# Performance work log

Measured on AMD Instinct MI355X. Metric: run time of the kernel, lower is better.

Reference implementation:

```python
import jax, jax.numpy as jnp
import numpy as np

F_, H_, W_ = 6, 16, 28          # latent video grid (frames, height, width)
DIM, NH = 1536, 12
HD = DIM // NH                   # 128
L = F_ * H_ * W_                 # 2688 tokens
EPS = 1e-6
BLOCK = 3 * H_ * W_              # block_causal_size = 3*frame_height*frame_width


def setup_inputs() -> dict:
    key = jax.random.key(0)
    ks = jax.random.split(key, 8)
    def lin(k):
        return jax.random.normal(k, (DIM, DIM), jnp.float32) * 0.02
    x = jax.random.normal(ks[0], (1, L, DIM), jnp.float32)
    # RoPE freqs: unit-modulus complex numbers stored as [...,(re,im)]
    ang = jax.random.uniform(ks[1], (1024, HD // 2), jnp.float32, -np.pi, np.pi)
    freqs = jnp.stack([jnp.cos(ang), jnp.sin(ang)], axis=-1)  # [1024, 64, 2]
    return {
        'x': x,
        'seq_lens': jnp.array([L], jnp.int32),
        'grid_sizes': jnp.array([[F_, H_, W_]], jnp.int32),
        'freqs': freqs,
        'Wq': lin(ks[2]), 'bq': jnp.zeros((DIM,), jnp.float32),
        'Wk': lin(ks[3]), 'bk': jnp.zeros((DIM,), jnp.float32),
        'Wv': lin(ks[4]), 'bv': jnp.zeros((DIM,), jnp.float32),
        'Wo': lin(ks[5]), 'bo': jnp.zeros((DIM,), jnp.float32),
        'gq': jnp.ones((DIM,), jnp.float32),
        'gk': jnp.ones((DIM,), jnp.float32),
    }


def _rmsnorm(x, g):
    # WanRMSNorm: x * rsqrt(mean(x^2) + eps) * weight
    return x * jax.lax.rsqrt(jnp.mean(x * x, axis=-1, keepdims=True) + EPS) * g


def _rope_apply(x, F, H, W, freqs, start_frame=0):
    # x: [B, L, n, d]; freqs: [1024, d//2, 2] (re, im). Per-axis split [c0, c3, c3].
    B, Lx, n, d = x.shape
    c = d // 2
    c3 = c // 3
    c0 = c - 2 * c3
    f0 = freqs[start_frame:start_frame + F, :c0]      # [F, c0, 2]
    f1 = freqs[:H, c0:c0 + c3]                        # [H, c3, 2]
    f2 = freqs[:W, c0 + c3:]                          # [W, c3, 2]
    ff = jnp.concatenate([
        jnp.broadcast_to(f0[:, None, None], (F, H, W, c0, 2)),
        jnp.broadcast_to(f1[None, :, None], (F, H, W, c3, 2)),
        jnp.broadcast_to(f2[None, None, :], (F, H, W, c3, 2)),
    ], axis=3).reshape(Lx, 1, c, 2)                   # [L, 1, c, 2]
    xr = x.reshape(B, Lx, n, c, 2)
    xre, xim = xr[..., 0], xr[..., 1]
    fre, fim = ff[None, ..., 0], ff[None, ..., 1]     # broadcast over batch, heads
    ore = xre * fre - xim * fim
    oim = xre * fim + xim * fre
    return jnp.stack([ore, oim], axis=-1).reshape(B, Lx, n, d)


def reference(x, seq_lens, grid_sizes, freqs, Wq, bq, Wk, bk, Wv, bv, Wo, bo, gq, gk):
    b, s = x.shape[:2]
    F = int(grid_sizes[0, 0]); H = int(grid_sizes[0, 1]); W = int(grid_sizes[0, 2])
    q = _rmsnorm(x @ Wq + bq, gq).reshape(b, s, NH, HD)
    k = _rmsnorm(x @ Wk + bk, gk).reshape(b, s, NH, HD)
    v = (x @ Wv + bv).reshape(b, s, NH, HD)
    rq = _rope_apply(q, F, H, W, freqs)
    rk = _rope_apply(k, F, H, W, freqs)
    # block-causal attention: query attends to keys in same-or-earlier 3-frame block
    scores = jnp.einsum('bihd,bjhd->bhij', rq, rk) * (HD ** -0.5)
    blk = jnp.arange(s) // (3 * H * W)
    mask = blk[None, :] <= blk[:, None]               # [s, s]
    scores = jnp.where(mask[None, None], scores, -1e30)
    attn = jax.nn.softmax(scores, axis=-1)
    out = jnp.einsum('bhij,bjhd->bihd', attn, v).reshape(b, s, DIM)
    return out @ Wo + bo
```

## Files before the change

kernel.cpp:

```cpp
#include <hip/hip_runtime.h>

#define L_SEQ 2688
#define DIM   1536
#define NH    12
#define HD    128
#define BLK_TOK 1344
#define HW_   448
#define W_    28

typedef unsigned short u16;
typedef unsigned int   u32;
typedef __attribute__((ext_vector_type(4))) float f32x4;
typedef __attribute__((ext_vector_type(16))) float f32x16;
typedef __attribute__((ext_vector_type(8))) short s16x8;
typedef __attribute__((ext_vector_type(2))) int i32x2;
typedef __attribute__((ext_vector_type(4))) u32 u32x4;

__device__ __forceinline__ u16 f2b(float f) {
    u32 u = __builtin_bit_cast(u32, f);
    return (u16)((u + 0x7FFFu + ((u >> 16) & 1u)) >> 16);
}
__device__ __forceinline__ float b2f(u16 b) {
    return __builtin_bit_cast(float, (u32)b << 16);
}
__device__ __forceinline__ u32 cvt_pk_bf16(float lo, float hi) {
    u32 r;
    asm("v_cvt_pk_bf16_f32 %0, %1, %2" : "=v"(r) : "v"(lo), "v"(hi));
    return r;
}

__global__ __launch_bounds__(256) void k_cvt_x(const float* __restrict__ x,
                                               u16* __restrict__ xb, int n4) {
    int i = blockIdx.x * 256 + threadIdx.x;
    int stride = gridDim.x * 256;
    for (; i < n4; i += stride) {
        float4 v = ((const float4*)x)[i];
        ushort4 o;
        o.x = f2b(v.x); o.y = f2b(v.y); o.z = f2b(v.z); o.w = f2b(v.w);
        ((ushort4*)xb)[i] = o;
    }
}

__global__ __launch_bounds__(256) void k_trans_w(const float* __restrict__ w0,
                                                 const float* __restrict__ w1,
                                                 const float* __restrict__ w2,
                                                 const float* __restrict__ w3,
                                                 u16* __restrict__ wt_all) {
    const float* w = blockIdx.z == 0 ? w0 : blockIdx.z == 1 ? w1 : blockIdx.z == 2 ? w2 : w3;
    u16* wt = wt_all + (size_t)blockIdx.z * DIM * DIM;
    __shared__ float t[64][65];
    const int k0 = blockIdx.y * 64, n0 = blockIdx.x * 64;
    const int c = threadIdx.x & 63, rg = threadIdx.x >> 6;
#pragma unroll
    for (int it = 0; it < 16; ++it) {
        int r = rg * 16 + it;
        t[r][c] = w[(size_t)(k0 + r) * DIM + n0 + c];
    }
    __syncthreads();
#pragma unroll
    for (int it = 0; it < 16; ++it) {
        int r = rg * 16 + it;
        wt[(size_t)(n0 + r) * DIM + k0 + c] = f2b(t[c][r]);
    }
}

template<int OUTF>
__global__ __launch_bounds__(256, 2) void k_gemm(const u16* __restrict__ A,
                                                 const u16* __restrict__ Bt_all,
                                                 const float* __restrict__ b0,
                                                 const float* __restrict__ b1,
                                                 const float* __restrict__ b2,
                                                 void* __restrict__ out_all) {
    const int z = blockIdx.z;
    const u16* Bt = Bt_all + (size_t)z * DIM * DIM;
    const float* bias = z == 0 ? b0 : z == 1 ? b1 : b2;

    __shared__ u16 lA[128 * 32];
    __shared__ u16 lB[128 * 32];
    const int tid = threadIdx.x, lane = tid & 63, wid = tid >> 6;
    const int wm = wid >> 1, wn = wid & 1;
    const int bm = blockIdx.y, bn = blockIdx.x;
    const int lr = lane & 15, lg = lane >> 4;

    f32x4 acc[4][4] = {};

    for (int kt = 0; kt < DIM / 32; ++kt) {
#pragma unroll
        for (int i = 0; i < 2; ++i) {
            int s = wid * 128 + i * 64 + lane;
            int row = s >> 2, c16 = s & 3;
            const u16* ga = A + (size_t)(bm * 128 + row) * DIM + kt * 32 + c16 * 8;
            __builtin_amdgcn_global_load_lds(
                (const __attribute__((address_space(1))) u32*)ga,
                (__attribute__((address_space(3))) u32*)&lA[(wid * 128 + i * 64) * 8],
                16, 0, 0);
            const u16* gb = Bt + (size_t)(bn * 128 + row) * DIM + kt * 32 + c16 * 8;
            __builtin_amdgcn_global_load_lds(
                (const __attribute__((address_space(1))) u32*)gb,
                (__attribute__((address_space(3))) u32*)&lB[(wid * 128 + i * 64) * 8],
                16, 0, 0);
        }
        __syncthreads();
        s16x8 af[4], bf[4];
#pragma unroll
        for (int m = 0; m < 4; ++m)
            af[m] = *(const s16x8*)&lA[(wm * 64 + m * 16 + lr) * 32 + lg * 8];
#pragma unroll
        for (int n = 0; n < 4; ++n)
            bf[n] = *(const s16x8*)&lB[(wn * 64 + n * 16 + lr) * 32 + lg * 8];
#pragma unroll
        for (int m = 0; m < 4; ++m)
#pragma unroll
            for (int n = 0; n < 4; ++n)
                acc[m][n] = __builtin_amdgcn_mfma_f32_16x16x32_bf16(af[m], bf[n], acc[m][n], 0, 0, 0);
        __syncthreads();
    }
#pragma unroll
    for (int n = 0; n < 4; ++n) {
        int col = bn * 128 + wn * 64 + n * 16 + lr;
        float bv = bias[col];
#pragma unroll
        for (int m = 0; m < 4; ++m) {
            int row0 = bm * 128 + wm * 64 + m * 16 + lg * 4;
#pragma unroll
            for (int r = 0; r < 4; ++r) {
                float v = acc[m][n][r] + bv;
                if (OUTF)
                    ((float*)out_all)[(size_t)(row0 + r) * DIM + col] = v;
                else
                    ((u16*)out_all)[(size_t)z * L_SEQ * DIM + (size_t)(row0 + r) * DIM + col] = f2b(v);
            }
        }
    }
}

__global__ __launch_bounds__(256) void k_norm_rope(const u16* __restrict__ pre_all,
                                                   const float* __restrict__ gq,
                                                   const float* __restrict__ gk,
                                                   const float* __restrict__ freqs,
                                                   u16* __restrict__ qh,
                                                   u16* __restrict__ kh) {
    const int which = blockIdx.y;
    const u16* pre = pre_all + (size_t)which * L_SEQ * DIM;
    const float* g = which ? gk : gq;
    u16* outh = which ? kh : qh;

    const int i = blockIdx.x;
    const int t = threadIdx.x;
    const u32* prow = (const u32*)(pre + (size_t)i * DIM);

    float re[3], im[3];
    float ss = 0.f;
#pragma unroll
    for (int a = 0; a < 3; ++a) {
        u32 p = prow[t + a * 256];
        float x = b2f((u16)(p & 0xFFFFu)), y = b2f((u16)(p >> 16));
        re[a] = x; im[a] = y;
        ss += x * x + y * y;
    }
#pragma unroll
    for (int o = 32; o > 0; o >>= 1) ss += __shfl_down(ss, o, 64);
    __shared__ float sred[4];
    if ((t & 63) == 0) sred[t >> 6] = ss;
    __syncthreads();
    float rms = rsqrtf((sred[0] + sred[1] + sred[2] + sred[3]) * (1.0f / DIM) + 1e-6f);

    const int f = i / HW_;
    const int rem = i - f * HW_;
    const int hp = rem / W_;
    const int wp = rem - hp * W_;
#pragma unroll
    for (int a = 0; a < 3; ++a) {
        int j = t + a * 256;
        int h = j >> 6, pj = j & 63;
        float2 gg = ((const float2*)g)[j];
        float x = re[a] * rms * gg.x;
        float y = im[a] * rms * gg.y;
        int ridx = pj < 22 ? f : (pj < 43 ? hp : wp);
        float2 cs = ((const float2*)freqs)[ridx * 64 + pj];
        float ore = x * cs.x - y * cs.y;
        float oim = x * cs.y + y * cs.x;
        u32 o = (u32)f2b(ore) | ((u32)f2b(oim) << 16);
        ((u32*)outh)[(size_t)h * (L_SEQ * 64) + (size_t)i * 64 + pj] = o;
    }
}

__global__ __launch_bounds__(256) void k_vtrans(const u16* __restrict__ vpre,
                                                u16* __restrict__ vt) {
    const int i0 = blockIdx.x * 64, d0 = blockIdx.y * 64, h = blockIdx.z;
    __shared__ u16 t[64][68];
    const int c = threadIdx.x & 63, rg = threadIdx.x >> 6;
#pragma unroll
    for (int it = 0; it < 16; ++it) {
        int r = rg * 16 + it;
        t[r][c] = vpre[(size_t)(i0 + r) * DIM + h * HD + d0 + c];
    }
    __syncthreads();
#pragma unroll
    for (int it = 0; it < 16; ++it) {
        int r = rg * 16 + it;
        vt[(size_t)h * (HD * L_SEQ) + (size_t)(d0 + r) * L_SEQ + i0 + c] = t[c][r];
    }
}

__global__ __launch_bounds__(256, 2) void k_attn(const u16* __restrict__ qh,
                                                 const u16* __restrict__ kh,
                                                 const u16* __restrict__ vt,
                                                 u16* __restrict__ ob,
                                                 float* __restrict__ Opart,
                                                 float* __restrict__ mlp) {
    __shared__ char lsm[2][32768];

    const int flat = blockIdx.x;
    const int xcd = flat & 7, idx = flat >> 3;
    const int work = (xcd < 4) ? (xcd * 95 + idx) : (380 + (xcd - 4) * 94 + idx);
    const int head = work / 63;
    const int bx = work - head * 63;
    int qt, kv0, mode;
    if (bx < 21)      { qt = bx;      kv0 = 0;  mode = 0; }
    else if (bx < 42) { qt = bx;      kv0 = 0;  mode = 1; }
    else              { qt = bx - 21; kv0 = 21; mode = 2; }

    const int tid = threadIdx.x, lane = tid & 63, w = tid >> 6;
    const int pairI = w >> 1;
    const int qhalf = w & 1;
    const int q31 = lane & 31, hi = lane >> 5;
    const size_t hOff = (size_t)head * ((size_t)L_SEQ * HD);
    const u16* Kh = kh + hOff;
    const u16* Vh = vt + hOff;
    const int qrow0 = qt * 64 + qhalf * 32;

    s16x8 aq[8];
#pragma unroll
    for (int kk = 0; kk < 8; ++kk)
        aq[kk] = *(const s16x8*)&qh[hOff + (size_t)(qrow0 + q31) * HD + kk * 16 + hi * 8];

    const int pt = tid & 127;
    const int rh = pt >> 4, ck = pt & 15;
    const int rv = pt >> 3, cvv = pt & 7;
    char* slot = lsm[pairI];

    f32x16 acc[4] = {};
    float mrun = -1e30f, lrun = 0.f;
    const float sc2 = 0.12751739646917983f;

    for (int it = 0; it < 11; ++it) {
        const int mytile = 2 * it + pairI;
        const bool active = mytile < 21;
        if (active) {
            const int tg = kv0 + mytile;
#pragma unroll
            for (int i = 0; i < 8; ++i) {
                const u16* src = Kh + (size_t)(tg * 64 + i * 8 + rh) * HD + 8 * (ck ^ ((i & 1) * 8 + rh));
                __builtin_amdgcn_global_load_lds(
                    (const __attribute__((address_space(1))) u32*)src,
                    (__attribute__((address_space(3))) u32*)(slot + i * 2048 + pt * 16), 16, 0, 0);
            }
#pragma unroll
            for (int i = 0; i < 8; ++i) {
                const u16* src = Vh + (size_t)(i * 16 + rv) * L_SEQ + tg * 64 + 8 * (cvv ^ (rv & 7));
                __builtin_amdgcn_global_load_lds(
                    (const __attribute__((address_space(1))) u32*)src,
                    (__attribute__((address_space(3))) u32*)(slot + 16384 + i * 2048 + pt * 16), 16, 0, 0);
            }
        }
        __syncthreads();
        if (active) {
            f32x16 sv[2] = {};
            __builtin_amdgcn_s_setprio(1);
#pragma unroll
            for (int js = 0; js < 2; ++js)
#pragma unroll
                for (int kk = 0; kk < 8; ++kk) {
                    int off = (js * 32 + q31) * 256 + ((kk * 32 + hi * 16) ^ ((q31 & 15) << 4));
                    s16x8 kf = *(const s16x8*)(slot + off);
                    sv[js] = __builtin_amdgcn_mfma_f32_32x32x16_bf16(kf, aq[kk], sv[js], 0, 0, 0);
                }
            __builtin_amdgcn_s_setprio(0);

            float mx = fmaxf(sv[0][0], sv[1][0]);
#pragma unroll
            for (int e = 1; e < 16; ++e) mx = fmaxf(mx, fmaxf(sv[0][e], sv[1][e]));
            mx = fmaxf(mx, __shfl_xor(mx, 32, 64));
            mx *= sc2;
            const int resc = (mx - mrun) > 11.5f;
            const float mm = resc ? mx : mrun;
            const float fac = resc ? __builtin_amdgcn_exp2f(mrun - mm) : 1.0f;
            mrun = mm;
            float sum = 0.f;
#pragma unroll
            for (int js = 0; js < 2; ++js)
#pragma unroll
                for (int e = 0; e < 16; ++e) {
                    float pv = __builtin_amdgcn_exp2f(sv[js][e] * sc2 - mm);
                    sv[js][e] = pv;
                    sum += pv;
                }
            sum += __shfl_xor(sum, 32, 64);
            lrun = lrun * fac + sum;
            if (__any(resc)) {
#pragma unroll
                for (int ds = 0; ds < 4; ++ds)
#pragma unroll
                    for (int e = 0; e < 16; ++e) acc[ds][e] *= fac;
            }

            s16x8 pa[4];
#pragma unroll
            for (int js = 0; js < 2; ++js)
#pragma unroll
                for (int hf = 0; hf < 2; ++hf) {
                    u32 a0 = cvt_pk_bf16(sv[js][hf * 8 + 0], sv[js][hf * 8 + 1]);
                    u32 a1 = cvt_pk_bf16(sv[js][hf * 8 + 2], sv[js][hf * 8 + 3]);
                    u32 b0 = cvt_pk_bf16(sv[js][hf * 8 + 4], sv[js][hf * 8 + 5]);
                    u32 b1 = cvt_pk_bf16(sv[js][hf * 8 + 6], sv[js][hf * 8 + 7]);
                    i32x2 r0 = __builtin_amdgcn_permlane32_swap((int)a0, (int)b0, false, false);
                    i32x2 r1 = __builtin_amdgcn_permlane32_swap((int)a1, (int)b1, false, false);
                    u32x4 fw;
                    fw.x = (u32)r0.x; fw.y = (u32)r1.x; fw.z = (u32)r0.y; fw.w = (u32)r1.y;
                    pa[js * 2 + hf] = __builtin_bit_cast(s16x8, fw);
                }

            __builtin_amdgcn_s_setprio(1);
#pragma unroll
            for (int jstep = 0; jstep < 4; ++jstep)
#pragma unroll
                for (int ds = 0; ds < 4; ++ds) {
                    int off = 16384 + (ds * 32 + q31) * 128 + ((jstep * 32 + hi * 16) ^ ((q31 & 7) << 4));
                    s16x8 vf = *(const s16x8*)(slot + off);
                    acc[ds] = __builtin_amdgcn_mfma_f32_32x32x16_bf16(vf, pa[jstep], acc[ds], 0, 0, 0);
                }
            __builtin_amdgcn_s_setprio(0);
        }
        __syncthreads();
    }

    float2* mlb = (float2*)(lsm[1]);
    char* accb = lsm[0];
    if (w >= 2) {
        char* base = accb + qhalf * 16384 + lane * 256;
#pragma unroll
        for (int ds = 0; ds < 4; ++ds)
#pragma unroll
            for (int g = 0; g < 4; ++g) {
                f32x4 v4;
#pragma unroll
                for (int e = 0; e < 4; ++e) v4[e] = acc[ds][g * 4 + e];
                *(f32x4*)(base + (((ds * 4 + g) * 16) ^ ((lane & 15) << 4))) = v4;
            }
        if (hi == 0) {
            float2 t2; t2.x = mrun; t2.y = lrun;
            mlb[qhalf * 32 + q31] = t2;
        }
    }
    __syncthreads();
    if (w < 2) {
        float2 ml2 = mlb[qhalf * 32 + q31];
        float M = fmaxf(mrun, ml2.x);
        float wa = exp2f(mrun - M), wb = exp2f(ml2.x - M);
        lrun = lrun * wa + ml2.y * wb;
        mrun = M;
        const char* base = accb + qhalf * 16384 + lane * 256;
#pragma unroll
        for (int ds = 0; ds < 4; ++ds)
#pragma unroll
            for (int g = 0; g < 4; ++g) {
                f32x4 v4 = *(const f32x4*)(base + (((ds * 4 + g) * 16) ^ ((lane & 15) << 4)));
#pragma unroll
                for (int e = 0; e < 4; ++e) acc[ds][g * 4 + e] = acc[ds][g * 4 + e] * wa + v4[e] * wb;
            }
        if (mode == 0) {
            const float inv = 1.0f / lrun;
            u16* orow = ob + (size_t)(qrow0 + q31) * DIM + head * HD;
#pragma unroll
            for (int ds = 0; ds < 4; ++ds)
#pragma unroll
                for (int g = 0; g < 4; ++g) {
                    uint2 pk2;
                    pk2.x = cvt_pk_bf16(acc[ds][g * 4 + 0] * inv, acc[ds][g * 4 + 1] * inv);
                    pk2.y = cvt_pk_bf16(acc[ds][g * 4 + 2] * inv, acc[ds][g * 4 + 3] * inv);
                    *(uint2*)(orow + ds * 32 + g * 8 + hi * 4) = pk2;
                }
        } else {
            const int pairo = (head * 21 + (qt - 21)) * 2 + (mode - 1);
            float* Op = Opart + (size_t)pairo * (64 * 128);
            const int rowl = qhalf * 32 + q31;
#pragma unroll
            for (int ds = 0; ds < 4; ++ds)
#pragma unroll
                for (int g = 0; g < 4; ++g) {
                    float4 v4;
                    v4.x = acc[ds][g * 4 + 0]; v4.y = acc[ds][g * 4 + 1];
                    v4.z = acc[ds][g * 4 + 2]; v4.w = acc[ds][g * 4 + 3];
                    *(float4*)(&Op[rowl * 128 + ds * 32 + g * 8 + hi * 4]) = v4;
                }
            if (hi == 0) {
                float2 t2; t2.x = mrun; t2.y = lrun;
                ((float2*)mlp)[(size_t)pairo * 64 + rowl] = t2;
            }
        }
    }
}

__global__ __launch_bounds__(256) void k_merge(const float* __restrict__ Opart,
                                               const float* __restrict__ mlp,
                                               u16* __restrict__ ob) {
    const int b = blockIdx.x;
    const int qt2 = b % 21, head = b / 21;
    const int pair = head * 21 + qt2;
    const float* O0 = Opart + (size_t)pair * 2 * 8192;
    const float* O1 = O0 + 8192;
    const int tid = threadIdx.x;
    const int row = tid >> 2, cs = (tid & 3) * 32;
    float2 a = ((const float2*)mlp)[(size_t)pair * 2 * 64 + row];
    float2 c = ((const float2*)mlp)[(size_t)(pair * 2 + 1) * 64 + row];
    float M = fmaxf(a.x, c.x);
    float w0 = exp2f(a.x - M), w1 = exp2f(c.x - M);
    float inv = 1.0f / (w0 * a.y + w1 * c.y);
    w0 *= inv; w1 *= inv;
    const int rowg = BLK_TOK + qt2 * 64 + row;
    u32* orow = (u32*)(ob + (size_t)rowg * DIM + head * HD + cs);
    const float4* p0 = (const float4*)(O0 + row * 128 + cs);
    const float4* p1 = (const float4*)(O1 + row * 128 + cs);
#pragma unroll
    for (int u = 0; u < 8; ++u) {
        float4 x0 = p0[u], x1 = p1[u];
        float o0 = x0.x * w0 + x1.x * w1;
        float o1 = x0.y * w0 + x1.y * w1;
        float o2 = x0.z * w0 + x1.z * w1;
        float o3 = x0.w * w0 + x1.w * w1;
        orow[u * 2]     = (u32)f2b(o0) | ((u32)f2b(o1) << 16);
        orow[u * 2 + 1] = (u32)f2b(o2) | ((u32)f2b(o3) << 16);
    }
}

extern "C" void kernel_launch(void* const* d_in, const int* in_sizes, int n_in,
                              void* d_out, int out_size, void* d_ws, size_t ws_size,
                              hipStream_t stream) {
    const float* x     = (const float*)d_in[0];
    const float* freqs = (const float*)d_in[3];
    const float* Wq    = (const float*)d_in[4];
    const float* bq    = (const float*)d_in[5];
    const float* Wk    = (const float*)d_in[6];
    const float* bk    = (const float*)d_in[7];
    const float* Wv    = (const float*)d_in[8];
    const float* bv    = (const float*)d_in[9];
    const float* Wo    = (const float*)d_in[10];
    const float* bo    = (const float*)d_in[11];
    const float* gq    = (const float*)d_in[12];
    const float* gk    = (const float*)d_in[13];

    const size_t LD = (size_t)L_SEQ * DIM;
    u16* wt_all  = (u16*)d_ws;
    u16* xb      = wt_all + (size_t)4 * DIM * DIM;
    u16* pre_all = xb + LD;
    u16* qh      = pre_all + 3 * LD;
    u16* kh2     = qh + LD;
    u16* vt      = kh2 + LD;
    u16* ob      = vt + LD;
    float* Opart = (float*)pre_all;
    float* mlp   = Opart + (size_t)12 * 21 * 2 * 64 * 128;

    k_cvt_x<<<2016, 256, 0, stream>>>(x, xb, (int)(LD / 4));
    k_trans_w<<<dim3(24, 24, 4), 256, 0, stream>>>(Wq, Wk, Wv, Wo, wt_all);
    k_gemm<0><<<dim3(12, 21, 3), 256, 0, stream>>>(xb, wt_all, bq, bk, bv, pre_all);
    k_norm_rope<<<dim3(L_SEQ, 2), 256, 0, stream>>>(pre_all, gq, gk, freqs, qh, kh2);
    k_vtrans<<<dim3(42, 2, NH), 256, 0, stream>>>(pre_all + 2 * LD, vt);
    k_attn<<<dim3(756), 256, 0, stream>>>(qh, kh2, vt, ob, Opart, mlp);
    k_merge<<<dim3(252), 256, 0, stream>>>(Opart, mlp, ob);
    k_gemm<1><<<dim3(12, 21, 1), 256, 0, stream>>>(ob, wt_all + (size_t)3 * DIM * DIM, bo, bo, bo, d_out);
}
```

Baseline: 173.7 us.

## Process two query tiles per attention workgroup to reuse K/V tiles

Restructures the attention kernel so each workgroup handles two 64-row query tiles, with each wave computing 64 query rows (two 32-row halves) against every K/V tile it loads into LDS. This halves the number of workgroups and the K/V global-to-LDS traffic per query. In exchange it doubles accumulator and Q fragment register pressure per wave, and with 11 pairs per context the last pair has an idle half. The grid shrinks to 396 blocks, which may leave CUs underused.

```diff
diff --git a/kernel.cpp b/kernel.cpp
--- a/kernel.cpp
+++ b/kernel.cpp
@@ -203,6 +203,51 @@
     }
 }
 
+__device__ __forceinline__ void softmax_pack(f32x16* sv, float& mrun, float& lrun,
+                                             f32x16* acc, s16x8* pa) {
+    const float sc2 = 0.12751739646917983f;
+    float mx = fmaxf(sv[0][0], sv[1][0]);
+#pragma unroll
+    for (int e = 1; e < 16; ++e) mx = fmaxf(mx, fmaxf(sv[0][e], sv[1][e]));
+    mx = fmaxf(mx, __shfl_xor(mx, 32, 64));
+    mx *= sc2;
+    const int resc = (mx - mrun) > 11.5f;
+    const float mm = resc ? mx : mrun;
+    const float fac = resc ? __builtin_amdgcn_exp2f(mrun - mm) : 1.0f;
+    mrun = mm;
+    float sum = 0.f;
+#pragma unroll
+    for (int js = 0; js < 2; ++js)
+#pragma unroll
+        for (int e = 0; e < 16; ++e) {
+            float pv = __builtin_amdgcn_exp2f(sv[js][e] * sc2 - mm);
+            sv[js][e] = pv;
+            sum += pv;
+        }
+    sum += __shfl_xor(sum, 32, 64);
+    lrun = lrun * fac + sum;
+    if (__any(resc)) {
+#pragma unroll
+        for (int ds = 0; ds < 4; ++ds)
+#pragma unroll
+            for (int e = 0; e < 16; ++e) acc[ds][e] *= fac;
+    }
+#pragma unroll
+    for (int js = 0; js < 2; ++js)
+#pragma unroll
+        for (int hf = 0; hf < 2; ++hf) {
+            u32 a0 = cvt_pk_bf16(sv[js][hf * 8 + 0], sv[js][hf * 8 + 1]);
+            u32 a1 = cvt_pk_bf16(sv[js][hf * 8 + 2], sv[js][hf * 8 + 3]);
+            u32 b0 = cvt_pk_bf16(sv[js][hf * 8 + 4], sv[js][hf * 8 + 5]);
+            u32 b1 = cvt_pk_bf16(sv[js][hf * 8 + 6], sv[js][hf * 8 + 7]);
+            i32x2 r0 = __builtin_amdgcn_permlane32_swap((int)a0, (int)b0, false, false);
+            i32x2 r1 = __builtin_amdgcn_permlane32_swap((int)a1, (int)b1, false, false);
+            u32x4 fw;
+            fw.x = (u32)r0.x; fw.y = (u32)r1.x; fw.z = (u32)r0.y; fw.w = (u32)r1.y;
+            pa[js * 2 + hf] = __builtin_bit_cast(s16x8, fw);
+        }
+}
+
 __global__ __launch_bounds__(256, 2) void k_attn(const u16* __restrict__ qh,
                                                  const u16* __restrict__ kh,
                                                  const u16* __restrict__ vt,
@@ -210,44 +255,48 @@
                                                  float* __restrict__ Opart,
                                                  float* __restrict__ mlp) {
     __shared__ char lsm[2][32768];
+    __shared__ float2 mlb2[2][64];
 
     const int flat = blockIdx.x;
     const int xcd = flat & 7, idx = flat >> 3;
-    const int work = (xcd < 4) ? (xcd * 95 + idx) : (380 + (xcd - 4) * 94 + idx);
-    const int head = work / 63;
-    const int bx = work - head * 63;
-    int qt, kv0, mode;
-    if (bx < 21)      { qt = bx;      kv0 = 0;  mode = 0; }
-    else if (bx < 42) { qt = bx;      kv0 = 0;  mode = 1; }
-    else              { qt = bx - 21; kv0 = 21; mode = 2; }
+    const int work = (xcd < 4) ? (xcd * 50 + idx) : (200 + (xcd - 4) * 49 + idx);
+    const int head = work / 33;
+    const int rem = work - head * 33;
+    const int ctx = rem / 11, p = rem - (rem / 11) * 11;
+    const int qbase = (ctx == 0) ? 0 : 21;
+    const int kv0 = (ctx == 2) ? 21 : 0;
+    const int mode = ctx;
 
     const int tid = threadIdx.x, lane = tid & 63, w = tid >> 6;
-    const int pairI = w >> 1;
-    const int qhalf = w & 1;
+    const int P = w >> 1, S = w & 1;
     const int q31 = lane & 31, hi = lane >> 5;
+    const int qt = qbase + 2 * p + S;
+    const bool qvalid = (2 * p + S) < 21;
+
     const size_t hOff = (size_t)head * ((size_t)L_SEQ * HD);
     const u16* Kh = kh + hOff;
     const u16* Vh = vt + hOff;
-    const int qrow0 = qt * 64 + qhalf * 32;
-
-    s16x8 aq[8];
-#pragma unroll
-    for (int kk = 0; kk < 8; ++kk)
-        aq[kk] = *(const s16x8*)&qh[hOff + (size_t)(qrow0 + q31) * HD + kk * 16 + hi * 8];
+
+    s16x8 aq0[8], aq1[8];
+    const u16* qp = qh + hOff + (size_t)(qt * 64 + q31) * HD + hi * 8;
+#pragma unroll
+    for (int kk = 0; kk < 8; ++kk) {
+        aq0[kk] = *(const s16x8*)(qp + kk * 16);
+        aq1[kk] = *(const s16x8*)(qp + (size_t)32 * HD + kk * 16);
+    }
 
     const int pt = tid & 127;
     const int rh = pt >> 4, ck = pt & 15;
     const int rv = pt >> 3, cvv = pt & 7;
-    char* slot = lsm[pairI];
-
-    f32x16 acc[4] = {};
-    float mrun = -1e30f, lrun = 0.f;
-    const float sc2 = 0.12751739646917983f;
+    char* slot = lsm[P];
+
+    f32x16 acc0[4] = {}, acc1[4] = {};
+    float mrun0 = -1e30f, lrun0 = 0.f, mrun1 = -1e30f, lrun1 = 0.f;
 
     for (int it = 0; it < 11; ++it) {
-        const int mytile = 2 * it + pairI;
-        const bool active = mytile < 21;
-        if (active) {
+        const int mytile = 2 * it + P;
+        const bool tact = mytile < 21;
+        if (tact) {
             const int tg = kv0 + mytile;
 #pragma unroll
             for (int i = 0; i < 8; ++i) {
@@ -265,8 +314,8 @@
             }
         }
         __syncthreads();
-        if (active) {
-            f32x16 sv[2] = {};
+        if (tact && qvalid) {
+            f32x16 sva[2] = {}, svb[2] = {};
             __builtin_amdgcn_s_setprio(1);
 #pragma unroll
             for (int js = 0; js < 2; ++js)
@@ -274,52 +323,14 @@
                 for (int kk = 0; kk < 8; ++kk) {
                     int off = (js * 32 + q31) * 256 + ((kk * 32 + hi * 16) ^ ((q31 & 15) << 4));
                     s16x8 kf = *(const s16x8*)(slot + off);
-                    sv[js] = __builtin_amdgcn_mfma_f32_32x32x16_bf16(kf, aq[kk], sv[js], 0, 0, 0);
+                    sva[js] = __builtin_amdgcn_mfma_f32_32x32x16_bf16(kf, aq0[kk], sva[js], 0, 0, 0);
+                    svb[js] = __builtin_amdgcn_mfma_f32_32x32x16_bf16(kf, aq1[kk], svb[js], 0, 0, 0);
                 }
             __builtin_amdgcn_s_setprio(0);
 
-            float mx = fmaxf(sv[0][0], sv[1][0]);
-#pragma unroll
-            for (int e = 1; e < 16; ++e) mx = fmaxf(mx, fmaxf(sv[0][e], sv[1][e]));
-            mx = fmaxf(mx, __shfl_xor(mx, 32, 64));
-            mx *= sc2;
-            const int resc = (mx - mrun) > 11.5f;
-            const float mm = resc ? mx : mrun;
-            const float fac = resc ? __builtin_amdgcn_exp2f(mrun - mm) : 1.0f;
-            mrun = mm;
-            float sum = 0.f;
-#pragma unroll
-            for (int js = 0; js < 2; ++js)
-#pragma unroll
-                for (int e = 0; e < 16; ++e) {
-                    float pv = __builtin_amdgcn_exp2f(sv[js][e] * sc2 - mm);
-                    sv[js][e] = pv;
-                    sum += pv;
-                }
-            sum += __shfl_xor(sum, 32, 64);
-            lrun = lrun * fac + sum;
-            if (__any(resc)) {
-#pragma unroll
-                for (int ds = 0; ds < 4; ++ds)
-#pragma unroll
-                    for (int e = 0; e < 16; ++e) acc[ds][e] *= fac;
-            }
-
-            s16x8 pa[4];
-#pragma unroll
-            for (int js = 0; js < 2; ++js)
-#pragma unroll
-                for (int hf = 0; hf < 2; ++hf) {
-                    u32 a0 = cvt_pk_bf16(sv[js][hf * 8 + 0], sv[js][hf * 8 + 1]);
-                    u32 a1 = cvt_pk_bf16(sv[js][hf * 8 + 2], sv[js][hf * 8 + 3]);
-                    u32 b0 = cvt_pk_bf16(sv[js][hf * 8 + 4], sv[js][hf * 8 + 5]);
-                    u32 b1 = cvt_pk_bf16(sv[js][hf * 8 + 6], sv[js][hf * 8 + 7]);
-                    i32x2 r0 = __builtin_amdgcn_permlane32_swap((int)a0, (int)b0, false, false);
-                    i32x2 r1 = __builtin_amdgcn_permlane32_swap((int)a1, (int)b1, false, false);
-                    u32x4 fw;
-                    fw.x = (u32)r0.x; fw.y = (u32)r1.x; fw.z = (u32)r0.y; fw.w = (u32)r1.y;
-                    pa[js * 2 + hf] = __builtin_bit_cast(s16x8, fw);
-                }
+            s16x8 pa0[4], pa1[4];
+            softmax_pack(sva, mrun0, lrun0, acc0, pa0);
+            softmax_pack(svb, mrun1, lrun1, acc1, pa1);
 
             __builtin_amdgcn_s_setprio(1);
 #pragma unroll
@@ -328,75 +339,87 @@
                 for (int ds = 0; ds < 4; ++ds) {
                     int off = 16384 + (ds * 32 + q31) * 128 + ((jstep * 32 + hi * 16) ^ ((q31 & 7) << 4));
                     s16x8 vf = *(const s16x8*)(slot + off);
-                    acc[ds] = __builtin_amdgcn_mfma_f32_32x32x16_bf16(vf, pa[jstep], acc[ds], 0, 0, 0);
+                    acc0[ds] = __builtin_amdgcn_mfma_f32_32x32x16_bf16(vf, pa0[jstep], acc0[ds], 0, 0, 0);
+                    acc1[ds] = __builtin_amdgcn_mfma_f32_32x32x16_bf16(vf, pa1[jstep], acc1[ds], 0, 0, 0);
                 }
             __builtin_amdgcn_s_setprio(0);
         }
         __syncthreads();
     }
 
-    float2* mlb = (float2*)(lsm[1]);
-    char* accb = lsm[0];
-    if (w >= 2) {
-        char* base = accb + qhalf * 16384 + lane * 256;
+    char* lsmc = (char*)lsm;
+    if (P == 1 && qvalid) {
+        char* base = lsmc + S * 32768 + lane * 512;
 #pragma unroll
         for (int ds = 0; ds < 4; ++ds)
 #pragma unroll
-            for (int g = 0; g < 4; ++g) {
-                f32x4 v4;
-#pragma unroll
-                for (int e = 0; e < 4; ++e) v4[e] = acc[ds][g * 4 + e];
-                *(f32x4*)(base + (((ds * 4 + g) * 16) ^ ((lane & 15) << 4))) = v4;
+            for (int g4 = 0; g4 < 4; ++g4) {
+                f32x4 v0, v1;
+#pragma unroll
+                for (int e = 0; e < 4; ++e) { v0[e] = acc0[ds][g4 * 4 + e]; v1[e] = acc1[ds][g4 * 4 + e]; }
+                int i0 = ds * 4 + g4, i1 = 16 + ds * 4 + g4;
+                *(f32x4*)(base + ((i0 * 16) ^ ((lane & 31) << 4))) = v0;
+                *(f32x4*)(base + ((i1 * 16) ^ ((lane & 31) << 4))) = v1;
             }
         if (hi == 0) {
-            float2 t2; t2.x = mrun; t2.y = lrun;
-            mlb[qhalf * 32 + q31] = t2;
+            float2 t0; t0.x = mrun0; t0.y = lrun0;
+            float2 t1; t1.x = mrun1; t1.y = lrun1;
+            mlb2[S][q31] = t0;
+            mlb2[S][32 + q31] = t1;
         }
     }
     __syncthreads();
-    if (w < 2) {
-        float2 ml2 = mlb[qhalf * 32 + q31];
-        float M = fmaxf(mrun, ml2.x);
-        float wa = exp2f(mrun - M), wb = exp2f(ml2.x - M);
-        lrun = lrun * wa + ml2.y * wb;
-        mrun = M;
-        const char* base = accb + qhalf * 16384 + lane * 256;
-#pragma unroll
-        for (int ds = 0; ds < 4; ++ds)
-#pragma unroll
-            for (int g = 0; g < 4; ++g) {
-                f32x4 v4 = *(const f32x4*)(base + (((ds * 4 + g) * 16) ^ ((lane & 15) << 4)));
-#pragma unroll
-                for (int e = 0; e < 4; ++e) acc[ds][g * 4 + e] = acc[ds][g * 4 + e] * wa + v4[e] * wb;
-            }
-        if (mode == 0) {
-            const float inv = 1.0f / lrun;
-            u16* orow = ob + (size_t)(qrow0 + q31) * DIM + head * HD;
+    if (P == 0 && qvalid) {
+        const char* base = lsmc + S * 32768 + lane * 512;
+#pragma unroll
+        for (int G = 0; G < 2; ++G) {
+            f32x16* acc = G ? acc1 : acc0;
+            float mr = G ? mrun1 : mrun0;
+            float lr = G ? lrun1 : lrun0;
+            float2 ml = mlb2[S][G * 32 + q31];
+            float M = fmaxf(mr, ml.x);
+            float wa = exp2f(mr - M), wb = exp2f(ml.x - M);
+            float lfin = lr * wa + ml.y * wb;
 #pragma unroll
             for (int ds = 0; ds < 4; ++ds)
 #pragma unroll
-                for (int g = 0; g < 4; ++g) {
-                    uint2 pk2;
-                    pk2.x = cvt_pk_bf16(acc[ds][g * 4 + 0] * inv, acc[ds][g * 4 + 1] * inv);
-                    pk2.y = cvt_pk_bf16(acc[ds][g * 4 + 2] * inv, acc[ds][g * 4 + 3] * inv);
-                    *(uint2*)(orow + ds * 32 + g * 8 + hi * 4) = pk2;
+                for (int g4 = 0; g4 < 4; ++g4) {
+                    int idx = G * 16 + ds * 4 + g4;
+                    f32x4 v4 = *(const f32x4*)(base + ((idx * 16) ^ ((lane & 31) << 4)));
+#pragma unroll
+                    for (int e = 0; e < 4; ++e)
+                        acc[ds][g4 * 4 + e] = acc[ds][g4 * 4 + e] * wa + v4[e] * wb;
                 }
-        } else {
-            const int pairo = (head * 21 + (qt - 21)) * 2 + (mode - 1);
-            float* Op = Opart + (size_t)pairo * (64 * 128);
-            const int rowl = qhalf * 32 + q31;
-#pragma unroll
-            for (int ds = 0; ds < 4; ++ds)
-#pragma unroll
-                for (int g = 0; g < 4; ++g) {
-                    float4 v4;
-                    v4.x = acc[ds][g * 4 + 0]; v4.y = acc[ds][g * 4 + 1];
-                    v4.z = acc[ds][g * 4 + 2]; v4.w = acc[ds][g * 4 + 3];
-                    *(float4*)(&Op[rowl * 128 + ds * 32 + g * 8 + hi * 4]) = v4;
+            const int row = qt * 64 + G * 32 + q31;
+            if (mode == 0) {
+                const float inv = 1.0f / lfin;
+                u16* orow = ob + (size_t)row * DIM + head * HD;
+#pragma unroll
+                for (int ds = 0; ds < 4; ++ds)
+#pragma unroll
+                    for (int g4 = 0; g4 < 4; ++g4) {
+                        uint2 pk2;
+                        pk2.x = cvt_pk_bf16(acc[ds][g4 * 4 + 0] * inv, acc[ds][g4 * 4 + 1] * inv);
+                        pk2.y = cvt_pk_bf16(acc[ds][g4 * 4 + 2] * inv, acc[ds][g4 * 4 + 3] * inv);
+                        *(uint2*)(orow + ds * 32 + g4 * 8 + hi * 4) = pk2;
+                    }
+            } else {
+                const int pairo = (head * 21 + (qt - 21)) * 2 + (mode - 1);
+                float* Op = Opart + (size_t)pairo * (64 * 128);
+                const int rowl = G * 32 + q31;
+#pragma unroll
+                for (int ds = 0; ds < 4; ++ds)
+#pragma unroll
+                    for (int g4 = 0; g4 < 4; ++g4) {
+                        float4 v4;
+                        v4.x = acc[ds][g4 * 4 + 0]; v4.y = acc[ds][g4 * 4 + 1];
+                        v4.z = acc[ds][g4 * 4 + 2]; v4.w = acc[ds][g4 * 4 + 3];
+                        *(float4*)(&Op[rowl * 128 + ds * 32 + g4 * 8 + hi * 4]) = v4;
+                    }
+                if (hi == 0) {
+                    float2 t2; t2.x = M; t2.y = lfin;
+                    ((float2*)mlp)[(size_t)pairo * 64 + rowl] = t2;
                 }
-            if (hi == 0) {
-                float2 t2; t2.x = mrun; t2.y = lrun;
-                ((float2*)mlp)[(size_t)pairo * 64 + rowl] = t2;
             }
         }
     }
@@ -466,7 +489,7 @@
     k_gemm<0><<<dim3(12, 21, 3), 256, 0, stream>>>(xb, wt_all, bq, bk, bv, pre_all);
     k_norm_rope<<<dim3(L_SEQ, 2), 256, 0, stream>>>(pre_all, gq, gk, freqs, qh, kh2);
     k_vtrans<<<dim3(42, 2, NH), 256, 0, stream>>>(pre_all + 2 * LD, vt);
-    k_attn<<<dim3(756), 256, 0, stream>>>(qh, kh2, vt, ob, Opart, mlp);
+    k_attn<<<dim3(396), 256, 0, stream>>>(qh, kh2, vt, ob, Opart, mlp);
     k_merge<<<dim3(252), 256, 0, stream>>>(Opart, mlp, ob);
     k_gemm<1><<<dim3(12, 21, 1), 256, 0, stream>>>(ob, wt_all + (size_t)3 * DIM * DIM, bo, bo, bo, d_out);
 }
```

Measured after the change: 226.1 us. 30.2% more time.

## Stagger KV tile staging so one wave pair loads while the other computes

Applied to the files above, without the earlier changes.

The attention loop used to have both wave pairs load their K/V tiles, synchronise, then compute at the same time. It now runs a 21-phase ping-pong: one pair stages the next tile into its LDS slot while the other pair runs MFMA and softmax on the tile already staged, after a prologue that loads the first tile. The aim is to hide global-to-LDS load latency behind compute. In exchange, only one pair computes in each phase, so the number of serialized steps roughly doubles and less MFMA work runs in parallel inside a block.

```diff
diff --git a/kernel.cpp b/kernel.cpp
--- a/kernel.cpp
+++ b/kernel.cpp
@@ -240,32 +240,34 @@
     const int rv = pt >> 3, cvv = pt & 7;
     char* slot = lsm[pairI];
 
+#define STAGE_TILE(TG)                                                            \
+    {                                                                             \
+        _Pragma("unroll")                                                         \
+        for (int i = 0; i < 8; ++i) {                                             \
+            const u16* src = Kh + (size_t)((TG) * 64 + i * 8 + rh) * HD + 8 * (ck ^ ((i & 1) * 8 + rh)); \
+            __builtin_amdgcn_global_load_lds(                                     \
+                (const __attribute__((address_space(1))) u32*)src,                \
+                (__attribute__((address_space(3))) u32*)(slot + i * 2048 + pt * 16), 16, 0, 0); \
+        }                                                                         \
+        _Pragma("unroll")                                                         \
+        for (int i = 0; i < 8; ++i) {                                             \
+            const u16* src = Vh + (size_t)(i * 16 + rv) * L_SEQ + (TG) * 64 + 8 * (cvv ^ (rv & 7)); \
+            __builtin_amdgcn_global_load_lds(                                     \
+                (const __attribute__((address_space(1))) u32*)src,                \
+                (__attribute__((address_space(3))) u32*)(slot + 16384 + i * 2048 + pt * 16), 16, 0, 0); \
+        }                                                                         \
+    }
+
     f32x16 acc[4] = {};
     float mrun = -1e30f, lrun = 0.f;
     const float sc2 = 0.12751739646917983f;
 
-    for (int it = 0; it < 11; ++it) {
-        const int mytile = 2 * it + pairI;
-        const bool active = mytile < 21;
-        if (active) {
-            const int tg = kv0 + mytile;
-#pragma unroll
-            for (int i = 0; i < 8; ++i) {
-                const u16* src = Kh + (size_t)(tg * 64 + i * 8 + rh) * HD + 8 * (ck ^ ((i & 1) * 8 + rh));
-                __builtin_amdgcn_global_load_lds(
-                    (const __attribute__((address_space(1))) u32*)src,
-                    (__attribute__((address_space(3))) u32*)(slot + i * 2048 + pt * 16), 16, 0, 0);
-            }
-#pragma unroll
-            for (int i = 0; i < 8; ++i) {
-                const u16* src = Vh + (size_t)(i * 16 + rv) * L_SEQ + tg * 64 + 8 * (cvv ^ (rv & 7));
-                __builtin_amdgcn_global_load_lds(
-                    (const __attribute__((address_space(1))) u32*)src,
-                    (__attribute__((address_space(3))) u32*)(slot + 16384 + i * 2048 + pt * 16), 16, 0, 0);
-            }
-        }
-        __syncthreads();
-        if (active) {
+    if (pairI == 0) STAGE_TILE(kv0);
+    __syncthreads();
+    for (int ph = 1; ph <= 21; ++ph) {
+        const int pst = ph & 1;
+        if (pairI == pst && ph <= 20) STAGE_TILE(kv0 + ph);
+        if (pairI == (pst ^ 1)) {
             f32x16 sv[2] = {};
             __builtin_amdgcn_s_setprio(1);
 #pragma unroll
@@ -400,6 +402,7 @@
             }
         }
     }
+#undef STAGE_TILE
 }
 
 __global__ __launch_bounds__(256) void k_merge(const float* __restrict__ Opart,
```

Result: slower. 184.5 us (+6.2%).
